# Kernel tuning notes

Measured on AMD Instinct MI355X. Metric: run time of the kernel, lower is better.

## Reference

```python
import jax, jax.numpy as jnp
import numpy as np

N = 50000      # nodes / stations
E = 600000     # edges
IN = 16        # in_channels
ED = 8         # edge_dim
HID = 128      # hidden
H = 4          # heads
C = HID // H   # 32 per-head channels
EMB = HID // 2 # station embedding dim
FEAT = HID - EMB
SLOPE = 0.2    # GATv2 LeakyReLU negative slope


def setup_inputs() -> dict:
    key = jax.random.key(0)
    ks = jax.random.split(key, 32)
    r = lambda i, shape, s=0.05: (jax.random.normal(ks[i], shape, jnp.float32) * s)
    inp = {
        "x": jax.random.normal(ks[0], (N, IN), jnp.float32),
        "node_idx": jax.random.randint(ks[1], (N,), 0, N),
        "edge_index": jax.random.randint(ks[2], (2, E), 0, N),
        "edge_attr": jax.random.normal(ks[3], (E, ED), jnp.float32),
        # params
        "emb": r(4, (N, EMB)),
        "W_in": r(5, (IN, FEAT)), "b_in": jnp.zeros((FEAT,), jnp.float32),
        # conv1 (GATv2: lin_l, lin_r, lin_edge, att, out bias)
        "Wl1": r(6, (HID, HID)), "bl1": jnp.zeros((HID,), jnp.float32),
        "Wr1": r(7, (HID, HID)), "br1": jnp.zeros((HID,), jnp.float32),
        "We1": r(8, (ED, HID)),  "be1": jnp.zeros((HID,), jnp.float32),
        "att1": r(9, (H, C)),    "bo1": jnp.zeros((HID,), jnp.float32),
        # conv2
        "Wl2": r(10, (HID, HID)), "bl2": jnp.zeros((HID,), jnp.float32),
        "Wr2": r(11, (HID, HID)), "br2": jnp.zeros((HID,), jnp.float32),
        "We2": r(12, (ED, HID)),  "be2": jnp.zeros((HID,), jnp.float32),
        "att2": r(13, (H, C)),    "bo2": jnp.zeros((HID,), jnp.float32),
        # layer norms
        "g1": jnp.ones((HID,), jnp.float32), "beta1": jnp.zeros((HID,), jnp.float32),
        "g2": jnp.ones((HID,), jnp.float32), "beta2": jnp.zeros((HID,), jnp.float32),
        # output head
        "W_out": r(14, (HID, 1)), "b_out": jnp.zeros((1,), jnp.float32),
    }
    return inp


def _gatv2(x, src, dst, ea, Wl, bl, Wr, br, We, be, att, bo):
    # x: [N,HID] -> per-head projections [N,H,C]
    xl = (x @ Wl + bl).reshape(-1, H, C)   # source transform
    xr = (x @ Wr + br).reshape(-1, H, C)   # target transform
    ee = (ea @ We + be).reshape(-1, H, C)  # edge transform [E,H,C]
    s = jax.nn.leaky_relu(xl[src] + xr[dst] + ee, SLOPE)  # [E,H,C]
    logit = jnp.einsum('ehc,hc->eh', s, att)              # [E,H]
    # segment softmax over destination node
    amax = jax.lax.stop_gradient(jax.ops.segment_max(logit, dst, num_segments=N))
    amax = jnp.where(jnp.isfinite(amax), amax, 0.0)
    ex = jnp.exp(logit - amax[dst])
    den = jax.ops.segment_sum(ex, dst, num_segments=N)
    alpha = ex / den[dst]                                  # [E,H]
    out = jax.ops.segment_sum(xl[src] * alpha[..., None], dst, num_segments=N)
    return out.reshape(-1, HID) + bo


def _ln(x, g, b):
    mu = x.mean(-1, keepdims=True)
    v = ((x - mu) ** 2).mean(-1, keepdims=True)
    return (x - mu) * jax.lax.rsqrt(v + 1e-5) * g + b


def reference(x, node_idx, edge_index, edge_attr, emb, W_in, b_in,
              Wl1, bl1, Wr1, br1, We1, be1, att1, bo1,
              Wl2, bl2, Wr2, br2, We2, be2, att2, bo2,
              g1, beta1, g2, beta2, W_out, b_out):
    src, dst = edge_index[0], edge_index[1]
    feat = jax.nn.relu(x @ W_in + b_in)                       # [N,FEAT]
    z = jnp.concatenate([feat, emb[node_idx]], axis=-1)       # [N,HID]
    h = jax.nn.relu(_gatv2(z, src, dst, edge_attr, Wl1, bl1, Wr1, br1, We1, be1, att1, bo1))
    z = _ln(z + h, g1, beta1)
    h = jax.nn.relu(_gatv2(z, src, dst, edge_attr, Wl2, bl2, Wr2, br2, We2, be2, att2, bo2))
    z = _ln(z + h, g2, beta2)
    return (z @ W_out + b_out).squeeze(-1)                    # [N]
```

## Files before the change

### kernel.cpp

```cpp
#include <hip/hip_runtime.h>
#include <hip/hip_bf16.h>

#define NN 50000
#define NE 600000
#define IND 16
#define EDD 8
#define HIDD 128
#define NH 4
#define CC 32
#define EMBD 64
#define FEATD 64
#define NB_SCAN ((NN + 255) / 256)

typedef __hip_bfloat16 bf16;
typedef __attribute__((ext_vector_type(8))) short bshort8;
typedef __attribute__((ext_vector_type(4))) float floatx4;
typedef __attribute__((ext_vector_type(2))) float f32x2;

__device__ __forceinline__ unsigned short f2bu(float f) {
    unsigned int u = __float_as_uint(f);
    u += 0x7fffu + ((u >> 16) & 1u);
    return (unsigned short)(u >> 16);
}

#if defined(__has_builtin)
#if __has_builtin(__builtin_amdgcn_fdot2_f32_bf16)
#define HAS_DOT2BF 1
#endif
#endif
#ifndef HAS_DOT2BF
#define HAS_DOT2BF 0
#endif

#if HAS_DOT2BF
typedef __attribute__((ext_vector_type(2))) __bf16 bfx2;
__device__ __forceinline__ float dot2bf(unsigned int a, unsigned int b, float c) {
    return __builtin_amdgcn_fdot2_f32_bf16(__builtin_bit_cast(bfx2, a),
                                           __builtin_bit_cast(bfx2, b), c, false);
}
#else
__device__ __forceinline__ float dot2bf(unsigned int a, unsigned int b, float c) {
    float a0 = __uint_as_float(a << 16), a1 = __uint_as_float(a & 0xffff0000u);
    float b0 = __uint_as_float(b << 16), b1 = __uint_as_float(b & 0xffff0000u);
    return __builtin_fmaf(a1, b1, __builtin_fmaf(a0, b0, c));
}
#endif

template <bool F32>
__device__ __forceinline__ float LD(const void* p, long long i) {
    if constexpr (F32) return ((const float*)p)[i];
    else return __bfloat162float(((const bf16*)p)[i]);
}

__device__ __forceinline__ bool is_f32(const int* cnt) { return *cnt > 8; }

__global__ void k_detinit(const unsigned short* __restrict__ x, int nhalf,
                          int* __restrict__ cnt, int* __restrict__ deg,
                          int* __restrict__ dcnt) {
    if (blockIdx.x == 0) {
        __shared__ int red[256];
        int hits = 0;
        for (int i = threadIdx.x; i < nhalf; i += 256)
            if ((x[i] & 0x7F80u) == 0x7F80u) hits++;
        red[threadIdx.x] = hits;
        __syncthreads();
        for (int o = 128; o; o >>= 1) {
            if (threadIdx.x < o) red[threadIdx.x] += red[threadIdx.x + o];
            __syncthreads();
        }
        if (threadIdx.x == 0) *cnt = red[0];
    } else {
        int gid = (blockIdx.x - 1) * 256 + threadIdx.x;
        if (gid < NN) deg[gid] = 0;
        if (blockIdx.x == 1 && threadIdx.x < 64) dcnt[threadIdx.x] = 0;
    }
}

__global__ void k_hist(const int* __restrict__ ei, int* __restrict__ deg, int* __restrict__ rank) {
    int e = blockIdx.x * blockDim.x + threadIdx.x;
    if (e < NE) rank[e] = atomicAdd(&deg[ei[NE + e]], 1);
}

__global__ void k_scan1(const int* __restrict__ deg, int* __restrict__ off,
                        int* __restrict__ bsum, int* __restrict__ dcnt,
                        int* __restrict__ rankd) {
    __shared__ int tile[256];
    __shared__ int lh[64];
    __shared__ int lbase[64];
    int t = threadIdx.x;
    int gid = blockIdx.x * 256 + t;
    if (t < 64) lh[t] = 0;
    __syncthreads();
    int v = (gid < NN) ? deg[gid] : 0;
    int b = 63 - min(v, 63);
    int lr = 0;
    if (gid < NN) lr = atomicAdd(&lh[b], 1);
    tile[t] = v;
    __syncthreads();
    if (t < 64) lbase[t] = lh[t] ? atomicAdd(&dcnt[t], lh[t]) : 0;
    #pragma unroll
    for (int o = 1; o < 256; o <<= 1) {
        int u = (t >= o) ? tile[t - o] : 0;
        __syncthreads();
        tile[t] += u;
        __syncthreads();
    }
    if (gid < NN) {
        off[gid] = tile[t] - v;
        rankd[gid] = lbase[b] + lr;
    }
    if (t == 255) bsum[blockIdx.x] = tile[255];
}
__global__ void k_scan2(int* __restrict__ bsum, int* __restrict__ dcnt,
                        int* __restrict__ dbase) {
    __shared__ int tile[256];
    __shared__ int d2[64];
    int t = threadIdx.x;
    int v = (t < NB_SCAN) ? bsum[t] : 0;
    tile[t] = v;
    int dv = (t < 64) ? dcnt[t] : 0;
    if (t < 64) d2[t] = dv;
    __syncthreads();
    #pragma unroll
    for (int o = 1; o < 256; o <<= 1) {
        int u = (t >= o) ? tile[t - o] : 0;
        __syncthreads();
        tile[t] += u;
        __syncthreads();
    }
    #pragma unroll
    for (int o = 1; o < 64; o <<= 1) {
        int u = (t >= o && t < 64) ? d2[t - o] : 0;
        __syncthreads();
        if (t < 64) d2[t] += u;
        __syncthreads();
    }
    if (t < NB_SCAN) bsum[t] = tile[t] - v;
    if (t < 64) dbase[t] = d2[t] - dv;
}
__global__ void k_scan3(int* __restrict__ off, const int* __restrict__ bsum,
                        const int* __restrict__ deg, const int* __restrict__ rankd,
                        const int* __restrict__ dbase, int* __restrict__ perm) {
    int gid = blockIdx.x * 256 + threadIdx.x;
    if (gid < NN) {
        off[gid] += bsum[blockIdx.x];
        int b = 63 - min(deg[gid], 63);
        perm[dbase[b] + rankd[gid]] = gid;
    }
    if (gid == 0) off[NN] = NE;
}

template <bool F32>
__device__ void fill_impl(const int* __restrict__ ei, const int* __restrict__ off,
                          const int* __restrict__ rank, int* __restrict__ esrc,
                          uint4* __restrict__ ea8, const void* ea) {
    int e = blockIdx.x * blockDim.x + threadIdx.x;
    if (e >= NE) return;
    if (e < 8) {
        esrc[NE + e] = 0;
        uint4 z; z.x = 0; z.y = 0; z.z = 0; z.w = 0;
        ea8[NE + e] = z;
    }
    int slot = off[ei[NE + e]] + rank[e];
    esrc[slot] = ei[e];
    uint4 v;
    if constexpr (F32) {
        const float4* ef = (const float4*)ea;
        float4 f0 = ef[2 * e], f1 = ef[2 * e + 1];
        v.x = (unsigned int)f2bu(f0.x) | ((unsigned int)f2bu(f0.y) << 16);
        v.y = (unsigned int)f2bu(f0.z) | ((unsigned int)f2bu(f0.w) << 16);
        v.z = (unsigned int)f2bu(f1.x) | ((unsigned int)f2bu(f1.y) << 16);
        v.w = (unsigned int)f2bu(f1.z) | ((unsigned int)f2bu(f1.w) << 16);
    } else {
        v = ((const uint4*)ea)[e];
    }
    ea8[slot] = v;
}
__global__ void k_fill(const int* cnt, const int* ei, const int* off, const int* rank,
                       int* esrc, uint4* ea8, const void* ea) {
    if (is_f32(cnt)) fill_impl<true>(ei, off, rank, esrc, ea8, ea);
    else             fill_impl<false>(ei, off, rank, esrc, ea8, ea);
}

template <bool F32>
__device__ void bzpw_impl(const void* x, const int* __restrict__ node_idx, const void* emb,
                          const void* W_in, const void* b_in, bf16* __restrict__ zb,
                          const void* Wl1, const void* bl1, const void* Wr1, const void* br1,
                          const void* Wl2, const void* bl2, const void* Wr2, const void* br2,
                          bf16* __restrict__ wbT, float* __restrict__ bias) {
    int t = threadIdx.x;
    if (blockIdx.x < NN) {
        int n = blockIdx.x;
        float val;
        if (t < FEATD) {
            float acc = LD<F32>(b_in, t);
            #pragma unroll
            for (int k = 0; k < IND; k++)
                acc += LD<F32>(x, (long long)n * IND + k) * LD<F32>(W_in, k * FEATD + t);
            val = fmaxf(acc, 0.f);
        } else {
            val = LD<F32>(emb, (long long)node_idx[n] * EMBD + (t - FEATD));
        }
        zb[n * HIDD + t] = __float2bfloat16(val);
    } else {
        int bid = blockIdx.x - NN;
        int layer = bid >> 8;
        int n = bid & 255;
        const void* W = layer ? (n < HIDD ? Wl2 : Wr2) : (n < HIDD ? Wl1 : Wr1);
        const void* b = layer ? (n < HIDD ? bl2 : br2) : (n < HIDD ? bl1 : br1);
        int nn = n & (HIDD - 1);
        wbT[(layer * 256 + n) * HIDD + t] = __float2bfloat16(LD<F32>(W, t * HIDD + nn));
        if (t == 0) bias[layer * 256 + n] = LD<F32>(b, nn);
    }
}
__global__ void k_bzpw(const int* cnt, const void* x, const int* node_idx, const void* emb,
                       const void* W_in, const void* b_in, bf16* zb,
                       const void* Wl1, const void* bl1, const void* Wr1, const void* br1,
                       const void* Wl2, const void* bl2, const void* Wr2, const void* br2,
                       bf16* wbT, float* bias) {
    if (is_f32(cnt)) bzpw_impl<true>(x, node_idx, emb, W_in, b_in, zb, Wl1, bl1, Wr1, br1,
                                     Wl2, bl2, Wr2, br2, wbT, bias);
    else             bzpw_impl<false>(x, node_idx, emb, W_in, b_in, zb, Wl1, bl1, Wr1, br1,
                                      Wl2, bl2, Wr2, br2, wbT, bias);
}

__global__ __launch_bounds__(256) void k_projmm(const bf16* __restrict__ zb,
                                                const bf16* __restrict__ wbT,
                                                const float* __restrict__ bias,
                                                bf16* __restrict__ xl, bf16* __restrict__ xr) {
    int wave = threadIdx.x >> 6, lane = threadIdx.x & 63;
    int m0 = blockIdx.x * 32;
    int n0 = wave * 64;
    int l15 = lane & 15, q = lane >> 4;
    bshort8 bfr[4][4];
    #pragma unroll
    for (int j = 0; j < 4; j++)
        #pragma unroll
        for (int s = 0; s < 4; s++)
            bfr[j][s] = *(const bshort8*)(wbT + ((n0 + j * 16 + l15) << 7) + s * 32 + q * 8);
    float bv[4];
    #pragma unroll
    for (int j = 0; j < 4; j++) bv[j] = bias[n0 + j * 16 + l15];
    const bf16* arow0 = zb + ((m0 + l15) << 7) + q * 8;
    const bf16* arow1 = arow0 + (16 << 7);
    bshort8 a0[4], a1[4];
    #pragma unroll
    for (int s = 0; s < 4; s++) a0[s] = *(const bshort8*)(arow0 + s * 32);
    #pragma unroll
    for (int s = 0; s < 4; s++) a1[s] = *(const bshort8*)(arow1 + s * 32);
    #pragma unroll
    for (int mi = 0; mi < 2; mi++) {
        floatx4 acc0 = {0.f, 0.f, 0.f, 0.f}, acc1 = acc0, acc2 = acc0, acc3 = acc0;
        #pragma unroll
        for (int s = 0; s < 4; s++) {
            bshort8 a = mi ? a1[s] : a0[s];
            acc0 = __builtin_amdgcn_mfma_f32_16x16x32_bf16(a, bfr[0][s], acc0, 0, 0, 0);
            acc1 = __builtin_amdgcn_mfma_f32_16x16x32_bf16(a, bfr[1][s], acc1, 0, 0, 0);
            acc2 = __builtin_amdgcn_mfma_f32_16x16x32_bf16(a, bfr[2][s], acc2, 0, 0, 0);
            acc3 = __builtin_amdgcn_mfma_f32_16x16x32_bf16(a, bfr[3][s], acc3, 0, 0, 0);
        }
        floatx4 accs[4] = {acc0, acc1, acc2, acc3};
        #pragma unroll
        for (int j = 0; j < 4; j++) {
            int colg = n0 + j * 16 + l15;
            bf16* dst = (colg < HIDD) ? (xl + colg) : (xr + (colg - HIDD));
            #pragma unroll
            for (int r = 0; r < 4; r++) {
                int rowc = m0 + mi * 16 + q * 4 + r;
                if (rowc < NN) dst[rowc << 7] = __float2bfloat16(accs[j][r] + bv[j]);
            }
        }
    }
}

__device__ __forceinline__ void edge_body(uint4 eu, uint2 xu, const unsigned int (*wp)[4],
                                          const float* base, const f32x2* at2,
                                          float mask, f32x2* acc, float& den) {
    f32x2 xv0, xv1;
    xv0.x = __uint_as_float(xu.x << 16); xv0.y = __uint_as_float(xu.x & 0xffff0000u);
    xv1.x = __uint_as_float(xu.y << 16); xv1.y = __uint_as_float(xu.y & 0xffff0000u);
    f32x2 e01, e23;
    {
        float c0 = base[0];
        c0 = dot2bf(eu.x, wp[0][0], c0);
        c0 = dot2bf(eu.y, wp[1][0], c0);
        c0 = dot2bf(eu.z, wp[2][0], c0);
        c0 = dot2bf(eu.w, wp[3][0], c0);
        float c1 = base[1];
        c1 = dot2bf(eu.x, wp[0][1], c1);
        c1 = dot2bf(eu.y, wp[1][1], c1);
        c1 = dot2bf(eu.z, wp[2][1], c1);
        c1 = dot2bf(eu.w, wp[3][1], c1);
        e01.x = c0; e01.y = c1;
        float c2 = base[2];
        c2 = dot2bf(eu.x, wp[0][2], c2);
        c2 = dot2bf(eu.y, wp[1][2], c2);
        c2 = dot2bf(eu.z, wp[2][2], c2);
        c2 = dot2bf(eu.w, wp[3][2], c2);
        float c3 = base[3];
        c3 = dot2bf(eu.x, wp[0][3], c3);
        c3 = dot2bf(eu.y, wp[1][3], c3);
        c3 = dot2bf(eu.z, wp[2][3], c3);
        c3 = dot2bf(eu.w, wp[3][3], c3);
        e23.x = c2; e23.y = c3;
    }
    f32x2 s0 = xv0 + e01;
    f32x2 s1 = xv1 + e23;
    s0 = __builtin_elementwise_max(s0, s0 * 0.2f);
    s1 = __builtin_elementwise_max(s1, s1 * 0.2f);
    f32x2 lsv = s0 * at2[0] + s1 * at2[1];
    float ls = lsv.x + lsv.y;
    ls += __shfl_xor(ls, 1);
    ls += __shfl_xor(ls, 2);
    ls += __shfl_xor(ls, 4);
    float ex = exp2f(ls) * mask;
    acc[0] += ex * xv0;
    acc[1] += ex * xv1;
    den += ex;
}

template <bool F32, bool LAST>
__device__ void gat_impl(const int* __restrict__ perm,
                         const int* __restrict__ off, const int* __restrict__ esrc,
                         const uint4* __restrict__ ea8,
                         const void* We, const void* be, const void* att,
                         const bf16* __restrict__ xl, const bf16* __restrict__ xr,
                         const void* bo, bf16* __restrict__ zb,
                         const void* g, const void* beta,
                         const void* Wo, const void* bout, void* out) {
    int wave = threadIdx.x >> 6;
    int half = (threadIdx.x >> 5) & 1;
    int lane5 = threadIdx.x & 31;
    int n = perm[blockIdx.x * 8 + wave * 2 + half];
    int c0 = lane5 << 2;
    unsigned int wp[4][4];
    #pragma unroll
    for (int p = 0; p < 4; p++)
        #pragma unroll
        for (int j = 0; j < 4; j++) {
            unsigned int lo = f2bu(LD<F32>(We, (2 * p) * HIDD + c0 + j));
            unsigned int hi = f2bu(LD<F32>(We, (2 * p + 1) * HIDD + c0 + j));
            wp[p][j] = lo | (hi << 16);
        }
    const float L2E = 1.4426950408889634f;
    f32x2 at2[2];
    at2[0].x = LD<F32>(att, c0 + 0) * L2E;
    at2[0].y = LD<F32>(att, c0 + 1) * L2E;
    at2[1].x = LD<F32>(att, c0 + 2) * L2E;
    at2[1].y = LD<F32>(att, c0 + 3) * L2E;
    uint2 xru = *(const uint2*)(xr + (n << 7) + c0);
    float xrv[4];
    xrv[0] = __uint_as_float(xru.x << 16);
    xrv[1] = __uint_as_float(xru.x & 0xffff0000u);
    xrv[2] = __uint_as_float(xru.y << 16);
    xrv[3] = __uint_as_float(xru.y & 0xffff0000u);
    float base[4];
    #pragma unroll
    for (int j = 0; j < 4; j++) base[j] = LD<F32>(be, c0 + j) + xrv[j];
    int lo = off[n], hi = off[n + 1];
    f32x2 accA[2] = {{0.f, 0.f}, {0.f, 0.f}}, accB[2] = {{0.f, 0.f}, {0.f, 0.f}};
    float denA = 0.f, denB = 0.f;
    if (lo < hi) {
        int sA = esrc[lo],      sB = esrc[lo + 1];
        uint4 eA = ea8[lo],     eB = ea8[lo + 1];
        int snA = esrc[lo + 2], snB = esrc[lo + 3];
        uint4 enA = ea8[lo + 2], enB = ea8[lo + 3];
        int s2A = esrc[lo + 4], s2B = esrc[lo + 5];
        uint4 e2A = ea8[lo + 4], e2B = ea8[lo + 5];
        uint2 xA = *(const uint2*)(xl + (sA << 7) + c0);
        uint2 xB = *(const uint2*)(xl + (sB << 7) + c0);
        uint2 xnA = *(const uint2*)(xl + (snA << 7) + c0);
        uint2 xnB = *(const uint2*)(xl + (snB << 7) + c0);
        for (int i = lo; i < hi; i += 2) {
            uint2 x2A = *(const uint2*)(xl + (s2A << 7) + c0);
            uint2 x2B = *(const uint2*)(xl + (s2B << 7) + c0);
            int s3A = esrc[i + 6],  s3B = esrc[i + 7];
            uint4 e3A = ea8[i + 6], e3B = ea8[i + 7];
            edge_body(eA, xA, wp, base, at2, 1.f, accA, denA);
            float mB = (i + 1 < hi) ? 1.f : 0.f;
            edge_body(eB, xB, wp, base, at2, mB, accB, denB);
            eA = enA; enA = e2A; e2A = e3A;
            eB = enB; enB = e2B; e2B = e3B;
            xA = xnA; xnA = x2A;
            xB = xnB; xnB = x2B;
            s2A = s3A; s2B = s3B;
        }
        accA[0] += accB[0];
        accA[1] += accB[1];
        denA += denB;
    }
    float inv = (denA > 0.f) ? 1.0f / denA : 0.f;
    uint2 zu = *(const uint2*)(zb + (n << 7) + c0);
    float zv[4];
    zv[0] = __uint_as_float(zu.x << 16);
    zv[1] = __uint_as_float(zu.x & 0xffff0000u);
    zv[2] = __uint_as_float(zu.y << 16);
    zv[3] = __uint_as_float(zu.y & 0xffff0000u);
    float accf[4] = {accA[0].x, accA[0].y, accA[1].x, accA[1].y};
    float v[4];
    float s = 0.f;
    #pragma unroll
    for (int j = 0; j < 4; j++) {
        float hv = fmaxf(accf[j] * inv + LD<F32>(bo, c0 + j), 0.f);
        v[j] = zv[j] + hv;
        s += v[j];
    }
    #pragma unroll
    for (int m = 16; m; m >>= 1) s += __shfl_xor(s, m);
    float mu = s * (1.f / HIDD);
    float s2 = 0.f;
    float dv[4];
    #pragma unroll
    for (int j = 0; j < 4; j++) { dv[j] = v[j] - mu; s2 += dv[j] * dv[j]; }
    #pragma unroll
    for (int m = 16; m; m >>= 1) s2 += __shfl_xor(s2, m);
    float rs = rsqrtf(s2 * (1.f / HIDD) + 1e-5f);
    float o[4];
    #pragma unroll
    for (int j = 0; j < 4; j++)
        o[j] = dv[j] * rs * LD<F32>(g, c0 + j) + LD<F32>(beta, c0 + j);
    if constexpr (!LAST) {
        uint2 pk;
        pk.x = (unsigned int)f2bu(o[0]) | ((unsigned int)f2bu(o[1]) << 16);
        pk.y = (unsigned int)f2bu(o[2]) | ((unsigned int)f2bu(o[3]) << 16);
        *(uint2*)(zb + (n << 7) + c0) = pk;
    } else {
        float po = 0.f;
        #pragma unroll
        for (int j = 0; j < 4; j++) po += o[j] * LD<F32>(Wo, c0 + j);
        #pragma unroll
        for (int m = 16; m; m >>= 1) po += __shfl_xor(po, m);
        if (lane5 == 0) {
            float r = po + LD<F32>(bout, 0);
            if constexpr (F32) ((float*)out)[n] = r;
            else               ((bf16*)out)[n] = __float2bfloat16(r);
        }
    }
}
__global__ void k_gat(const int* cnt, const int* perm, const int* off, const int* esrc,
                      const uint4* ea8, const void* We, const void* be, const void* att,
                      const bf16* xl, const bf16* xr, const void* bo, bf16* zb,
                      const void* g, const void* beta) {
    if (is_f32(cnt)) gat_impl<true, false>(perm, off, esrc, ea8, We, be, att, xl, xr, bo, zb, g, beta, nullptr, nullptr, nullptr);
    else             gat_impl<false, false>(perm, off, esrc, ea8, We, be, att, xl, xr, bo, zb, g, beta, nullptr, nullptr, nullptr);
}
__global__ void k_gat_last(const int* cnt, const int* perm, const int* off, const int* esrc,
                           const uint4* ea8, const void* We, const void* be, const void* att,
                           const bf16* xl, const bf16* xr, const void* bo, bf16* zb,
                           const void* g, const void* beta,
                           const void* Wo, const void* bout, void* out) {
    if (is_f32(cnt)) gat_impl<true, true>(perm, off, esrc, ea8, We, be, att, xl, xr, bo, zb, g, beta, Wo, bout, out);
    else             gat_impl<false, true>(perm, off, esrc, ea8, We, be, att, xl, xr, bo, zb, g, beta, Wo, bout, out);
}

extern "C" void kernel_launch(void* const* d_in, const int* in_sizes, int n_in,
                              void* d_out, int out_size, void* d_ws, size_t ws_size,
                              hipStream_t stream) {
    const void* x        = d_in[0];
    const int*  node_idx = (const int*)d_in[1];
    const int*  ei       = (const int*)d_in[2];
    const void* ea       = d_in[3];
    const void* emb      = d_in[4];
    const void* W_in     = d_in[5];
    const void* b_in     = d_in[6];
    const void* Wl1 = d_in[7];  const void* bl1 = d_in[8];
    const void* Wr1 = d_in[9];  const void* br1 = d_in[10];
    const void* We1 = d_in[11]; const void* be1 = d_in[12];
    const void* att1 = d_in[13]; const void* bo1 = d_in[14];
    const void* Wl2 = d_in[15]; const void* bl2 = d_in[16];
    const void* Wr2 = d_in[17]; const void* br2 = d_in[18];
    const void* We2 = d_in[19]; const void* be2 = d_in[20];
    const void* att2 = d_in[21]; const void* bo2 = d_in[22];
    const void* g1 = d_in[23]; const void* beta1 = d_in[24];
    const void* g2 = d_in[25]; const void* beta2 = d_in[26];
    const void* W_out = d_in[27]; const void* b_out = d_in[28];

    int*   cnt   = (int*)d_ws;
    uint4* ea8   = (uint4*)((char*)d_ws + 256);
    bf16*  zb    = (bf16*)(ea8 + NE + 8);
    bf16*  xl    = zb + NN * HIDD;
    bf16*  xr    = xl + NN * HIDD;
    bf16*  wbT   = xr + NN * HIDD;
    float* bias  = (float*)(wbT + 2 * 256 * HIDD);
    int*   off   = (int*)(bias + 512);
    int*   deg   = off + NN + 1;
    int*   rank  = deg + NN;
    int*   rankd = rank + NE;
    int*   perm  = rankd + NN;
    int*   esrc  = perm + NN;
    int*   bsum  = esrc + NE + 8;
    int*   dcnt  = bsum + 256;
    int*   dbase = dcnt + 64;

    int nhalf = in_sizes[0] < 16384 ? in_sizes[0] : 16384;
    k_detinit<<<NB_SCAN + 1, 256, 0, stream>>>((const unsigned short*)x, nhalf, cnt, deg, dcnt);
    k_hist<<<(NE + 255) / 256, 256, 0, stream>>>(ei, deg, rank);
    k_scan1<<<NB_SCAN, 256, 0, stream>>>(deg, off, bsum, dcnt, rankd);
    k_scan2<<<1, 256, 0, stream>>>(bsum, dcnt, dbase);
    k_scan3<<<NB_SCAN, 256, 0, stream>>>(off, bsum, deg, rankd, dbase, perm);
    k_bzpw<<<NN + 512, HIDD, 0, stream>>>(cnt, x, node_idx, emb, W_in, b_in, zb,
                                          Wl1, bl1, Wr1, br1, Wl2, bl2, Wr2, br2, wbT, bias);
    k_fill<<<(NE + 255) / 256, 256, 0, stream>>>(cnt, ei, off, rank, esrc, ea8, ea);

    k_projmm<<<(NN + 31) / 32, 256, 0, stream>>>(zb, wbT, bias, xl, xr);
    k_gat<<<NN / 8, 256, 0, stream>>>(cnt, perm, off, esrc, ea8, We1, be1, att1, xl, xr, bo1, zb, g1, beta1);

    k_projmm<<<(NN + 31) / 32, 256, 0, stream>>>(zb, wbT + 256 * HIDD, bias + 256, xl, xr);
    k_gat_last<<<NN / 8, 256, 0, stream>>>(cnt, perm, off, esrc, ea8, We2, be2, att2, xl, xr, bo2, zb,
                                           g2, beta2, W_out, b_out, d_out);
}
```

Before: 365.9 us.

## Deepen GAT edge prefetch pipeline and batch rows per block in setup and projection

```diff
diff --git a/kernel.cpp b/kernel.cpp
--- a/kernel.cpp
+++ b/kernel.cpp
@@ -11,6 +11,7 @@
 #define EMBD 64
 #define FEATD 64
 #define NB_SCAN ((NN + 255) / 256)
+#define NND8 (NN / 8)
 
 typedef __hip_bfloat16 bf16;
 typedef __attribute__((ext_vector_type(8))) short bshort8;
@@ -156,7 +157,7 @@
                           uint4* __restrict__ ea8, const void* ea) {
     int e = blockIdx.x * blockDim.x + threadIdx.x;
     if (e >= NE) return;
-    if (e < 8) {
+    if (e < 16) {
         esrc[NE + e] = 0;
         uint4 z; z.x = 0; z.y = 0; z.z = 0; z.w = 0;
         ea8[NE + e] = z;
@@ -189,21 +190,31 @@
                           const void* Wl2, const void* bl2, const void* Wr2, const void* br2,
                           bf16* __restrict__ wbT, float* __restrict__ bias) {
     int t = threadIdx.x;
-    if (blockIdx.x < NN) {
-        int n = blockIdx.x;
-        float val;
+    if (blockIdx.x < NND8) {
         if (t < FEATD) {
-            float acc = LD<F32>(b_in, t);
-            #pragma unroll
-            for (int k = 0; k < IND; k++)
-                acc += LD<F32>(x, (long long)n * IND + k) * LD<F32>(W_in, k * FEATD + t);
-            val = fmaxf(acc, 0.f);
+            float w[IND];
+            #pragma unroll
+            for (int k = 0; k < IND; k++) w[k] = LD<F32>(W_in, k * FEATD + t);
+            float bi = LD<F32>(b_in, t);
+            #pragma unroll 2
+            for (int nd = 0; nd < 8; nd++) {
+                int n = blockIdx.x * 8 + nd;
+                float acc = bi;
+                #pragma unroll
+                for (int k = 0; k < IND; k++)
+                    acc += LD<F32>(x, (long long)n * IND + k) * w[k];
+                zb[n * HIDD + t] = __float2bfloat16(fmaxf(acc, 0.f));
+            }
         } else {
-            val = LD<F32>(emb, (long long)node_idx[n] * EMBD + (t - FEATD));
-        }
-        zb[n * HIDD + t] = __float2bfloat16(val);
+            #pragma unroll 2
+            for (int nd = 0; nd < 8; nd++) {
+                int n = blockIdx.x * 8 + nd;
+                zb[n * HIDD + t] = __float2bfloat16(
+                    LD<F32>(emb, (long long)node_idx[n] * EMBD + (t - FEATD)));
+            }
+        }
     } else {
-        int bid = blockIdx.x - NN;
+        int bid = blockIdx.x - NND8;
         int layer = bid >> 8;
         int n = bid & 255;
         const void* W = layer ? (n < HIDD ? Wl2 : Wr2) : (n < HIDD ? Wl1 : Wr1);
@@ -229,7 +240,6 @@
                                                 const float* __restrict__ bias,
                                                 bf16* __restrict__ xl, bf16* __restrict__ xr) {
     int wave = threadIdx.x >> 6, lane = threadIdx.x & 63;
-    int m0 = blockIdx.x * 32;
     int n0 = wave * 64;
     int l15 = lane & 15, q = lane >> 4;
     bshort8 bfr[4][4];
@@ -241,33 +251,37 @@
     float bv[4];
     #pragma unroll
     for (int j = 0; j < 4; j++) bv[j] = bias[n0 + j * 16 + l15];
-    const bf16* arow0 = zb + ((m0 + l15) << 7) + q * 8;
-    const bf16* arow1 = arow0 + (16 << 7);
-    bshort8 a0[4], a1[4];
-    #pragma unroll
-    for (int s = 0; s < 4; s++) a0[s] = *(const bshort8*)(arow0 + s * 32);
-    #pragma unroll
-    for (int s = 0; s < 4; s++) a1[s] = *(const bshort8*)(arow1 + s * 32);
-    #pragma unroll
-    for (int mi = 0; mi < 2; mi++) {
-        floatx4 acc0 = {0.f, 0.f, 0.f, 0.f}, acc1 = acc0, acc2 = acc0, acc3 = acc0;
-        #pragma unroll
-        for (int s = 0; s < 4; s++) {
-            bshort8 a = mi ? a1[s] : a0[s];
-            acc0 = __builtin_amdgcn_mfma_f32_16x16x32_bf16(a, bfr[0][s], acc0, 0, 0, 0);
-            acc1 = __builtin_amdgcn_mfma_f32_16x16x32_bf16(a, bfr[1][s], acc1, 0, 0, 0);
-            acc2 = __builtin_amdgcn_mfma_f32_16x16x32_bf16(a, bfr[2][s], acc2, 0, 0, 0);
-            acc3 = __builtin_amdgcn_mfma_f32_16x16x32_bf16(a, bfr[3][s], acc3, 0, 0, 0);
-        }
-        floatx4 accs[4] = {acc0, acc1, acc2, acc3};
-        #pragma unroll
-        for (int j = 0; j < 4; j++) {
-            int colg = n0 + j * 16 + l15;
-            bf16* dst = (colg < HIDD) ? (xl + colg) : (xr + (colg - HIDD));
-            #pragma unroll
-            for (int r = 0; r < 4; r++) {
-                int rowc = m0 + mi * 16 + q * 4 + r;
-                if (rowc < NN) dst[rowc << 7] = __float2bfloat16(accs[j][r] + bv[j]);
+    #pragma unroll
+    for (int mt = 0; mt < 2; mt++) {
+        int m0 = blockIdx.x * 64 + mt * 32;
+        const bf16* arow0 = zb + ((m0 + l15) << 7) + q * 8;
+        const bf16* arow1 = arow0 + (16 << 7);
+        bshort8 a0[4], a1[4];
+        #pragma unroll
+        for (int s = 0; s < 4; s++) a0[s] = *(const bshort8*)(arow0 + s * 32);
+        #pragma unroll
+        for (int s = 0; s < 4; s++) a1[s] = *(const bshort8*)(arow1 + s * 32);
+        #pragma unroll
+        for (int mi = 0; mi < 2; mi++) {
+            floatx4 acc0 = {0.f, 0.f, 0.f, 0.f}, acc1 = acc0, acc2 = acc0, acc3 = acc0;
+            #pragma unroll
+            for (int s = 0; s < 4; s++) {
+                bshort8 a = mi ? a1[s] : a0[s];
+                acc0 = __builtin_amdgcn_mfma_f32_16x16x32_bf16(a, bfr[0][s], acc0, 0, 0, 0);
+                acc1 = __builtin_amdgcn_mfma_f32_16x16x32_bf16(a, bfr[1][s], acc1, 0, 0, 0);
+                acc2 = __builtin_amdgcn_mfma_f32_16x16x32_bf16(a, bfr[2][s], acc2, 0, 0, 0);
+                acc3 = __builtin_amdgcn_mfma_f32_16x16x32_bf16(a, bfr[3][s], acc3, 0, 0, 0);
+            }
+            floatx4 accs[4] = {acc0, acc1, acc2, acc3};
+            #pragma unroll
+            for (int j = 0; j < 4; j++) {
+                int colg = n0 + j * 16 + l15;
+                bf16* dst = (colg < HIDD) ? (xl + colg) : (xr + (colg - HIDD));
+                #pragma unroll
+                for (int r = 0; r < 4; r++) {
+                    int rowc = m0 + mi * 16 + q * 4 + r;
+                    if (rowc < NN) dst[rowc << 7] = __float2bfloat16(accs[j][r] + bv[j]);
+                }
             }
         }
     }
@@ -338,9 +352,9 @@
     for (int p = 0; p < 4; p++)
         #pragma unroll
         for (int j = 0; j < 4; j++) {
-            unsigned int lo = f2bu(LD<F32>(We, (2 * p) * HIDD + c0 + j));
-            unsigned int hi = f2bu(LD<F32>(We, (2 * p + 1) * HIDD + c0 + j));
-            wp[p][j] = lo | (hi << 16);
+            unsigned int lo_ = f2bu(LD<F32>(We, (2 * p) * HIDD + c0 + j));
+            unsigned int hi_ = f2bu(LD<F32>(We, (2 * p + 1) * HIDD + c0 + j));
+            wp[p][j] = lo_ | (hi_ << 16);
         }
     const float L2E = 1.4426950408889634f;
     f32x2 at2[2];
@@ -361,29 +375,40 @@
     f32x2 accA[2] = {{0.f, 0.f}, {0.f, 0.f}}, accB[2] = {{0.f, 0.f}, {0.f, 0.f}};
     float denA = 0.f, denB = 0.f;
     if (lo < hi) {
-        int sA = esrc[lo],      sB = esrc[lo + 1];
-        uint4 eA = ea8[lo],     eB = ea8[lo + 1];
-        int snA = esrc[lo + 2], snB = esrc[lo + 3];
-        uint4 enA = ea8[lo + 2], enB = ea8[lo + 3];
-        int s2A = esrc[lo + 4], s2B = esrc[lo + 5];
-        uint4 e2A = ea8[lo + 4], e2B = ea8[lo + 5];
-        uint2 xA = *(const uint2*)(xl + (sA << 7) + c0);
-        uint2 xB = *(const uint2*)(xl + (sB << 7) + c0);
-        uint2 xnA = *(const uint2*)(xl + (snA << 7) + c0);
-        uint2 xnB = *(const uint2*)(xl + (snB << 7) + c0);
-        for (int i = lo; i < hi; i += 2) {
-            uint2 x2A = *(const uint2*)(xl + (s2A << 7) + c0);
-            uint2 x2B = *(const uint2*)(xl + (s2B << 7) + c0);
-            int s3A = esrc[i + 6],  s3B = esrc[i + 7];
-            uint4 e3A = ea8[i + 6], e3B = ea8[i + 7];
-            edge_body(eA, xA, wp, base, at2, 1.f, accA, denA);
+        uint4 e0[4];
+        uint2 x0[4];
+        int s1[4];
+        #pragma unroll
+        for (int k = 0; k < 4; k++) {
+            int s = esrc[lo + k];
+            e0[k] = ea8[lo + k];
+            x0[k] = *(const uint2*)(xl + (s << 7) + c0);
+        }
+        #pragma unroll
+        for (int k = 0; k < 4; k++) s1[k] = esrc[lo + 4 + k];
+        for (int i = lo; i < hi; i += 4) {
+            uint2 xn[4];
+            uint4 e1[4];
+            int s2[4];
+            #pragma unroll
+            for (int k = 0; k < 4; k++) xn[k] = *(const uint2*)(xl + (s1[k] << 7) + c0);
+            #pragma unroll
+            for (int k = 0; k < 4; k++) e1[k] = ea8[i + 4 + k];
+            #pragma unroll
+            for (int k = 0; k < 4; k++) s2[k] = esrc[i + 8 + k];
+            edge_body(e0[0], x0[0], wp, base, at2, 1.f, accA, denA);
             float mB = (i + 1 < hi) ? 1.f : 0.f;
-            edge_body(eB, xB, wp, base, at2, mB, accB, denB);
-            eA = enA; enA = e2A; e2A = e3A;
-            eB = enB; enB = e2B; e2B = e3B;
-            xA = xnA; xnA = x2A;
-            xB = xnB; xnB = x2B;
-            s2A = s3A; s2B = s3B;
+            edge_body(e0[1], x0[1], wp, base, at2, mB, accB, denB);
+            float mC = (i + 2 < hi) ? 1.f : 0.f;
+            edge_body(e0[2], x0[2], wp, base, at2, mC, accA, denA);
+            float mD = (i + 3 < hi) ? 1.f : 0.f;
+            edge_body(e0[3], x0[3], wp, base, at2, mD, accB, denB);
+            #pragma unroll
+            for (int k = 0; k < 4; k++) {
+                e0[k] = e1[k];
+                x0[k] = xn[k];
+                s1[k] = s2[k];
+            }
         }
         accA[0] += accB[0];
         accA[1] += accB[1];
@@ -408,13 +433,13 @@
     #pragma unroll
     for (int m = 16; m; m >>= 1) s += __shfl_xor(s, m);
     float mu = s * (1.f / HIDD);
-    float s2 = 0.f;
+    float s2v = 0.f;
     float dv[4];
     #pragma unroll
-    for (int j = 0; j < 4; j++) { dv[j] = v[j] - mu; s2 += dv[j] * dv[j]; }
-    #pragma unroll
-    for (int m = 16; m; m >>= 1) s2 += __shfl_xor(s2, m);
-    float rs = rsqrtf(s2 * (1.f / HIDD) + 1e-5f);
+    for (int j = 0; j < 4; j++) { dv[j] = v[j] - mu; s2v += dv[j] * dv[j]; }
+    #pragma unroll
+    for (int m = 16; m; m >>= 1) s2v += __shfl_xor(s2v, m);
+    float rs = rsqrtf(s2v * (1.f / HIDD) + 1e-5f);
     float o[4];
     #pragma unroll
     for (int j = 0; j < 4; j++)
@@ -477,7 +502,7 @@
 
     int*   cnt   = (int*)d_ws;
     uint4* ea8   = (uint4*)((char*)d_ws + 256);
-    bf16*  zb    = (bf16*)(ea8 + NE + 8);
+    bf16*  zb    = (bf16*)(ea8 + NE + 16);
     bf16*  xl    = zb + NN * HIDD;
     bf16*  xr    = xl + NN * HIDD;
     bf16*  wbT   = xr + NN * HIDD;
@@ -488,7 +513,7 @@
     int*   rankd = rank + NE;
     int*   perm  = rankd + NN;
     int*   esrc  = perm + NN;
-    int*   bsum  = esrc + NE + 8;
+    int*   bsum  = esrc + NE + 16;
     int*   dcnt  = bsum + 256;
     int*   dbase = dcnt + 64;
 
@@ -498,14 +523,14 @@
     k_scan1<<<NB_SCAN, 256, 0, stream>>>(deg, off, bsum, dcnt, rankd);
     k_scan2<<<1, 256, 0, stream>>>(bsum, dcnt, dbase);
     k_scan3<<<NB_SCAN, 256, 0, stream>>>(off, bsum, deg, rankd, dbase, perm);
-    k_bzpw<<<NN + 512, HIDD, 0, stream>>>(cnt, x, node_idx, emb, W_in, b_in, zb,
-                                          Wl1, bl1, Wr1, br1, Wl2, bl2, Wr2, br2, wbT, bias);
+    k_bzpw<<<NND8 + 512, HIDD, 0, stream>>>(cnt, x, node_idx, emb, W_in, b_in, zb,
+                                            Wl1, bl1, Wr1, br1, Wl2, bl2, Wr2, br2, wbT, bias);
     k_fill<<<(NE + 255) / 256, 256, 0, stream>>>(cnt, ei, off, rank, esrc, ea8, ea);
 
-    k_projmm<<<(NN + 31) / 32, 256, 0, stream>>>(zb, wbT, bias, xl, xr);
+    k_projmm<<<(NN + 63) / 64, 256, 0, stream>>>(zb, wbT, bias, xl, xr);
     k_gat<<<NN / 8, 256, 0, stream>>>(cnt, perm, off, esrc, ea8, We1, be1, att1, xl, xr, bo1, zb, g1, beta1);
 
-    k_projmm<<<(NN + 31) / 32, 256, 0, stream>>>(zb, wbT + 256 * HIDD, bias + 256, xl, xr);
+    k_projmm<<<(NN + 63) / 64, 256, 0, stream>>>(zb, wbT + 256 * HIDD, bias + 256, xl, xr);
     k_gat_last<<<NN / 8, 256, 0, stream>>>(cnt, perm, off, esrc, ea8, We2, be2, att2, xl, xr, bo2, zb,
                                            g2, beta2, W_out, b_out, d_out);
 }
```

Result: no change. 364.1 us (-0.5%).
